# Kernel tuning notes

Measured on AMD Instinct MI355X. Metric: run time of the kernel, lower is better.

Reference implementation:

```python
import jax, jax.numpy as jnp
import numpy as np

B, CQ, CK, CV, CO = 16, 256, 256, 256, 256
H, W = 80, 80          # query spatial size (P3-like)
KH, KW = 40, 40        # key/value spatial size (P4-like)
HEADS = 4
R2 = 2 * 2             # region_size ** 2
SCALE = 1.0 / np.float32(np.sqrt(CQ))


def conv1x1(x, w, b):
    # 1x1 conv == per-pixel linear map over channels
    return jnp.einsum('bchw,oc->bohw', x, w) + b[None, :, None, None]


def setup_inputs() -> dict:
    key = jax.random.key(0)
    ks = jax.random.split(key, 10)
    s = 0.05
    return {
        'query': jax.random.normal(ks[0], (B, CQ, H, W), jnp.float32),
        'key':   jax.random.normal(ks[1], (B, CK, KH, KW), jnp.float32),
        'wq': jax.random.normal(ks[2], (CQ, CQ), jnp.float32) * s,
        'bq': jax.random.normal(ks[3], (CQ,), jnp.float32) * s,
        'wk': jax.random.normal(ks[4], (CK, CK), jnp.float32) * s,
        'bk': jax.random.normal(ks[5], (CK,), jnp.float32) * s,
        'wv': jax.random.normal(ks[6], (CV, CV), jnp.float32) * s,
        'bv': jax.random.normal(ks[7], (CV,), jnp.float32) * s,
        'wo': jax.random.normal(ks[8], (CO, CV), jnp.float32) * s,
        'bo': jax.random.normal(ks[9], (CO,), jnp.float32) * s,
    }


def reference(query, key, wq, bq, wk, bk, wv, bv, wo, bo):
    # value defaults to key in the original module
    q = conv1x1(query, wq, bq)               # [B,CQ,H,W]
    k = conv1x1(key, wk, bk)                 # [B,CK,KH,KW]
    v = conv1x1(key, wv, bv)                 # [B,CV,KH,KW]

    b, cq, h, w = q.shape
    # All R2 'patches' in the source are the SAME interpolation (no offsets),
    # so compute it once; bilinear resize matches torch align_corners=False.
    ki = jax.image.resize(k, (b, k.shape[1], h, w), method='bilinear')
    vi = jax.image.resize(v, (b, v.shape[1], h, w), method='bilinear')

    q5 = q.reshape(b, HEADS, cq // HEADS, h, w)
    k5 = ki.reshape(b, HEADS, k.shape[1] // HEADS, h, w)
    v5 = vi.reshape(b, HEADS, v.shape[1] // HEADS, h, w)

    # per-region score; identical for every region patch
    score = jnp.einsum('bhcxy,bhcxy->bhxy', q5, k5) * SCALE     # [B,h,H,W]
    scores = jnp.broadcast_to(score[:, :, None], (b, HEADS, R2, h, w))
    # NOTE: original uses nn.Softmax(dim=3) -> normalizes over the H axis
    attn = jax.nn.softmax(scores, axis=3)                       # [B,h,R2,H,W]

    # out = sum over regions of attn * v (v identical across regions)
    out = jnp.einsum('bhrxy,bhcxy->bhcxy', attn, v5)            # [B,h,C/h,H,W]
    out = out.reshape(b, -1, h, w)                              # [B,CV,H,W]
    return conv1x1(out, wo, bo)                                 # [B,CO,H,W]
```

## Files before the change

kernel.cpp:

```cpp
#include <hip/hip_runtime.h>
#include <hip/hip_bf16.h>

typedef __bf16 bf16;
typedef __attribute__((ext_vector_type(4))) float f32x4;
typedef __attribute__((ext_vector_type(8))) __bf16 bf16x8;
typedef __attribute__((ext_vector_type(4))) __bf16 bf16x4;

static __device__ __forceinline__ void gl16(const void* g, void* l) {
  __builtin_amdgcn_global_load_lds((const __attribute__((address_space(1))) void*)g,
                                   (__attribute__((address_space(3))) void*)l, 16, 0, 0);
}
static __device__ __forceinline__ bf16x8 frag(const bf16* tile, int row, int kb) {
  return *(const bf16x8*)(tile + row * 64 + ((((kb) >> 3) ^ (row & 7)) << 3));
}

__global__ void wpre(const float* __restrict__ w0, const float* __restrict__ w1,
                     const float* __restrict__ w2, const float* __restrict__ w3,
                     bf16* __restrict__ dst) {
  const float* srcs[4] = {w0, w1, w2, w3};
  const float* s = srcs[blockIdx.y];
  bf16* d = dst + (size_t)blockIdx.y * 65536;
  int base = blockIdx.x * 2048 + threadIdx.x * 8;
  f32x4 a = *(const f32x4*)(s + base);
  f32x4 b = *(const f32x4*)(s + base + 4);
  bf16x8 v = {(bf16)a[0], (bf16)a[1], (bf16)a[2], (bf16)a[3],
              (bf16)b[0], (bf16)b[1], (bf16)b[2], (bf16)b[3]};
  *(bf16x8*)(d + base) = v;
}

__global__ void wtr(const float* __restrict__ wq, bf16* __restrict__ wqT) {
  __shared__ float tl[64][65];
  const int r0 = blockIdx.x * 64, c0 = blockIdx.y * 64;
  const int t = threadIdx.x;
  const int cc = t & 63, rr = t >> 6;
#pragma unroll
  for (int i = 0; i < 16; ++i) {
    int r = i * 4 + rr;
    tl[r][cc] = wq[(size_t)(r0 + r) * 256 + c0 + cc];
  }
  __syncthreads();
#pragma unroll
  for (int i = 0; i < 16; ++i) {
    int r = i * 4 + rr;
    wqT[(size_t)(c0 + r) * 256 + r0 + cc] = (bf16)tl[cc][r];
  }
}

__global__ __launch_bounds__(256, 1)
void kv_proj(const float* __restrict__ key,
             const bf16* __restrict__ Wk, const float* __restrict__ bk, bf16* __restrict__ Kpm,
             const bf16* __restrict__ Wv, const float* __restrict__ bv, bf16* __restrict__ Vpm) {
  __shared__ alignas(16) char smem[64 * 264 * 2];
  const int P = 1600;
  const int t = threadIdx.x;
  const int b = blockIdx.z;
  const int p0 = blockIdx.x * 64;
  const int sel = blockIdx.y;
  const bf16* W = sel ? Wv : Wk;
  const float* bias = sel ? bv : bk;
  bf16* out = sel ? Vpm : Kpm;
  const int w = t >> 6, l = t & 63;
  const int lrow = l & 15, ksel = l >> 4;
  const int pq = t & 15, cq = t >> 4;
  const float* actb = key + (size_t)b * 256 * P;
  bf16* As = (bf16*)smem;

  f32x4 Ar[4][4];
#pragma unroll
  for (int kt = 0; kt < 4; ++kt)
#pragma unroll
    for (int j = 0; j < 4; ++j)
      Ar[kt][j] = *(const f32x4*)(actb + (size_t)(kt * 64 + cq * 4 + j) * P + p0 + pq * 4);
#pragma unroll
  for (int kt = 0; kt < 4; ++kt) {
    bf16* tile = As + kt * 4096;
#pragma unroll
    for (int e = 0; e < 4; ++e) {
      int row = pq * 4 + e;
      bf16x4 v = {(bf16)Ar[kt][0][e], (bf16)Ar[kt][1][e], (bf16)Ar[kt][2][e], (bf16)Ar[kt][3][e]};
      *(bf16x4*)(tile + row * 64 + ((((cq >> 1) ^ (row & 7)) << 3) | ((cq & 1) << 2))) = v;
    }
  }
  __syncthreads();

  f32x4 acc[4][4];
#pragma unroll
  for (int i = 0; i < 4; ++i)
#pragma unroll
    for (int j = 0; j < 4; ++j) acc[i][j] = (f32x4){0.f, 0.f, 0.f, 0.f};

#pragma unroll
  for (int kt = 0; kt < 4; ++kt) {
    const int k0 = kt * 64;
    const bf16* tile = As + kt * 4096;
    bf16x8 af[4][2], bv8[4][2];
#pragma unroll
    for (int mi = 0; mi < 4; ++mi)
#pragma unroll
      for (int kk = 0; kk < 2; ++kk)
        af[mi][kk] = *(const bf16x8*)(W + (size_t)(w * 64 + mi * 16 + lrow) * 256 +
                                      k0 + kk * 32 + ksel * 8);
#pragma unroll
    for (int ni = 0; ni < 4; ++ni)
#pragma unroll
      for (int kk = 0; kk < 2; ++kk)
        bv8[ni][kk] = frag(tile, ni * 16 + lrow, kk * 32 + ksel * 8);
#pragma unroll
    for (int kk = 0; kk < 2; ++kk)
#pragma unroll
      for (int mi = 0; mi < 4; ++mi)
#pragma unroll
        for (int ni = 0; ni < 4; ++ni)
          acc[mi][ni] = __builtin_amdgcn_mfma_f32_16x16x32_bf16(af[mi][kk], bv8[ni][kk],
                                                                acc[mi][ni], 0, 0, 0);
  }
  __syncthreads();

  bf16* Sc = (bf16*)smem;
#pragma unroll
  for (int mi = 0; mi < 4; ++mi) {
#pragma unroll
    for (int r = 0; r < 4; ++r) {
      int o = w * 64 + mi * 16 + ksel * 4 + r;
      float bvf = bias[o];
#pragma unroll
      for (int ni = 0; ni < 4; ++ni) {
        int px = ni * 16 + lrow;
        Sc[px * 264 + o] = (bf16)(acc[mi][ni][r] + bvf);
      }
    }
  }
  __syncthreads();
  bf16* ob = out + (size_t)b * P * 256 + (size_t)p0 * 256;
#pragma unroll
  for (int pass = 0; pass < 8; ++pass) {
    int idx = pass * 256 + t;
    int row = idx >> 5, cu = idx & 31;
    bf16x8 v = *(const bf16x8*)(Sc + row * 264 + cu * 8);
    *(bf16x8*)(ob + (size_t)row * 256 + cu * 8) = v;
  }
}

__global__ __launch_bounds__(256, 4)
void uv_gemm(const bf16* __restrict__ Bpm, const bf16* __restrict__ A,
             bf16* __restrict__ D) {
  __shared__ alignas(16) bf16 Vt[64 * 64];
  const int t = threadIdx.x;
  const int b = blockIdx.z;
  const int hd = blockIdx.y;
  const int q0 = blockIdx.x * 64;
  const int w = t >> 6, l = t & 63;
  const int lrow = l & 15, ksel = l >> 4;

  const bf16* vsrc = Bpm + ((size_t)b * 1600 + q0) * 256 + hd * 64;
#pragma unroll
  for (int call = 0; call < 2; ++call) {
    int idx = (w * 2 + call) * 64 + l;
    int q = idx >> 3, u = idx & 7;
    gl16(vsrc + (size_t)q * 256 + ((u ^ (q & 7)) << 3), Vt + idx * 8);
  }
  asm volatile("s_waitcnt vmcnt(0)" ::: "memory");
  __syncthreads();

  f32x4 acc[4][4];
#pragma unroll
  for (int i = 0; i < 4; ++i)
#pragma unroll
    for (int j = 0; j < 4; ++j) acc[i][j] = (f32x4){0.f, 0.f, 0.f, 0.f};

#pragma unroll
  for (int kk = 0; kk < 2; ++kk) {
    bf16x8 af[4], bv[4];
#pragma unroll
    for (int mi = 0; mi < 4; ++mi)
      af[mi] = *(const bf16x8*)(A + (size_t)(w * 64 + mi * 16 + lrow) * 256 +
                                hd * 64 + kk * 32 + ksel * 8);
#pragma unroll
    for (int ni = 0; ni < 4; ++ni)
      bv[ni] = frag(Vt, ni * 16 + lrow, kk * 32 + ksel * 8);
#pragma unroll
    for (int mi = 0; mi < 4; ++mi)
#pragma unroll
      for (int ni = 0; ni < 4; ++ni)
        acc[mi][ni] = __builtin_amdgcn_mfma_f32_16x16x32_bf16(af[mi], bv[ni], acc[mi][ni], 0, 0, 0);
  }

  bf16* ob = D + ((size_t)(b * 4 + hd)) * 256 * 1600;
#pragma unroll
  for (int mi = 0; mi < 4; ++mi) {
#pragma unroll
    for (int ni = 0; ni < 4; ++ni) {
#pragma unroll
      for (int r = 0; r < 4; ++r) {
        int o = w * 64 + mi * 16 + ksel * 4 + r;
        int q = q0 + ni * 16 + lrow;
        ob[(size_t)o * 1600 + q] = (bf16)acc[mi][ni][r];
      }
    }
  }
}

__global__ void beta_k(const bf16* __restrict__ Kpm, const float* __restrict__ bq,
                       bf16* __restrict__ beta) {
  __shared__ float bqs[256];
  const int t = threadIdx.x;
  bqs[t] = bq[t];
  __syncthreads();
  const int b = blockIdx.y;
  const int q = blockIdx.x * 64 + (t >> 2);
  const int hd = t & 3;
  const bf16* row = Kpm + ((size_t)b * 1600 + q) * 256 + hd * 64;
  float s = 0.f;
#pragma unroll
  for (int i = 0; i < 8; ++i) {
    bf16x8 v = *(const bf16x8*)(row + i * 8);
#pragma unroll
    for (int j = 0; j < 8; ++j) s += (float)v[j] * bqs[hd * 64 + i * 8 + j];
  }
  beta[((size_t)b * 4 + hd) * 1600 + q] = (bf16)s;
}

__global__ __launch_bounds__(256, 3)
void stream_score(const float* __restrict__ query, const bf16* __restrict__ T,
                  const bf16* __restrict__ beta, float* __restrict__ score) {
  __shared__ alignas(16) bf16 Tc[2][64][192];
  __shared__ bf16 Bs[4][192];
  const int t = threadIdx.x;
  const int p0 = blockIdx.x * 256;
  const int b = blockIdx.y;
  const int px = p0 + t;
  const int x = px / 80, y = px % 80;

  const int x_min = p0 / 80;
  int ixm = (int)floorf(0.5f * x_min - 0.25f);
  int xr0 = ixm < 0 ? 0 : ixm;
  int qbase = xr0 * 40;
  if (qbase > 1408) qbase = 1408;

  float cx = 0.5f * x - 0.25f;
  int ix = (int)floorf(cx);
  float wx1 = cx - ix;
  int x0 = ix < 0 ? 0 : ix, x1 = (ix + 1 > 39) ? 39 : ix + 1;
  float cy = 0.5f * y - 0.25f;
  int iy = (int)floorf(cy);
  float wy1 = cy - iy;
  int y0 = iy < 0 ? 0 : iy, y1 = (iy + 1 > 39) ? 39 : iy + 1;
  const float w00 = (1.f - wx1) * (1.f - wy1), w01 = (1.f - wx1) * wy1;
  const float w10 = wx1 * (1.f - wy1), w11 = wx1 * wy1;
  const int r00 = x0 * 40 + y0 - qbase, r01 = x0 * 40 + y1 - qbase;
  const int r10 = x1 * 40 + y0 - qbase, r11 = x1 * 40 + y1 - qbase;

  for (int i = t; i < 768; i += 256) {
    int hd = i / 192, qq = i - hd * 192;
    Bs[hd][qq] = beta[((size_t)b * 4 + hd) * 1600 + qbase + qq];
  }

  const bf16* Tb = T + (size_t)b * 4 * 256 * 1600;

  auto STAGE = [&](int c, int buf) {
    const int k0 = c * 16;
#pragma unroll
    for (int call = 0; call < 6; ++call) {
      int idx = call * 256 + t;
      int r = idx / 24, u = idx - r * 24;
      int hd = r >> 4, kk = r & 15;
      const bf16* src = Tb + ((size_t)(hd * 256) + k0 + kk) * 1600 + qbase + u * 8;
      gl16(src, &Tc[buf][0][0] + idx * 8);
    }
  };

  STAGE(0, 0);
  asm volatile("s_waitcnt vmcnt(0)" ::: "memory");
  __syncthreads();

  float acc[4];
#pragma unroll
  for (int hd = 0; hd < 4; ++hd)
    acc[hd] = w00 * (float)Bs[hd][r00] + w01 * (float)Bs[hd][r01] +
              w10 * (float)Bs[hd][r10] + w11 * (float)Bs[hd][r11];

  int buf = 0;
  for (int c = 0; c < 16; ++c) {
    if (c < 15) STAGE(c + 1, buf ^ 1);
    float qv[16];
#pragma unroll
    for (int kk = 0; kk < 16; ++kk)
      qv[kk] = query[((size_t)b * 256 + c * 16 + kk) * 6400 + px];
#pragma unroll
    for (int kk = 0; kk < 16; ++kk) {
#pragma unroll
      for (int hd = 0; hd < 4; ++hd) {
        const bf16* row = &Tc[buf][hd * 16 + kk][0];
        float tv = w00 * (float)row[r00] + w01 * (float)row[r01] +
                   w10 * (float)row[r10] + w11 * (float)row[r11];
        acc[hd] += qv[kk] * tv;
      }
    }
    asm volatile("s_waitcnt vmcnt(0)" ::: "memory");
    __syncthreads();
    buf ^= 1;
  }

#pragma unroll
  for (int hd = 0; hd < 4; ++hd)
    score[((size_t)b * 4 + hd) * 6400 + px] = 0.0625f * acc[hd];
}

__global__ void smax_kernel(float* __restrict__ score) {
  __shared__ float s[6400];
  const int hd = blockIdx.x, b = blockIdx.y, t = threadIdx.x;
  float* buf = score + ((size_t)b * 4 + hd) * 6400;
  for (int i = t; i < 6400; i += 256) s[i] = buf[i];
  __syncthreads();
  if (t < 80) {
    const int y = t;
    float m = -1e30f;
    for (int x = 0; x < 80; ++x) m = fmaxf(m, s[x * 80 + y]);
    float sum = 0.f;
    for (int x = 0; x < 80; ++x) {
      float e = __expf(s[x * 80 + y] - m);
      s[x * 80 + y] = e;
      sum += e;
    }
    float inv = 4.0f / sum;
    for (int x = 0; x < 80; ++x) buf[x * 80 + y] = s[x * 80 + y] * inv;
  }
}

__global__ __launch_bounds__(256, 8)
void combine(const bf16* __restrict__ Uv, const float* __restrict__ attn,
             const float* __restrict__ bo, float* __restrict__ out) {
  __shared__ bf16 Us[4][1600];
  __shared__ int   sx0[80], sx1[80];
  __shared__ float swx[80];
  const int t = threadIdx.x;
  const int o = blockIdx.x;
  const int b = blockIdx.y;

  const bf16* usrc = Uv + (size_t)(b * 4) * 256 * 1600 + (size_t)o * 1600;
  for (int idx = t; idx < 800; idx += 256) {
    int hd = idx / 200, u = idx % 200;
    *(bf16x8*)&Us[hd][u * 8] = *(const bf16x8*)(usrc + (size_t)hd * 256 * 1600 + u * 8);
  }
  if (t < 80) {
    float c = 0.5f * t - 0.25f;
    int i0 = (int)floorf(c);
    swx[t] = c - i0;
    sx0[t] = i0 < 0 ? 0 : i0;
    sx1[t] = (i0 + 1 > 39) ? 39 : i0 + 1;
  }
  __syncthreads();

  const float bias = bo[o];
  const float* attb = attn + (size_t)b * 4 * 6400;
  float* op = out + ((size_t)b * 256 + o) * 6400;

  for (int p = t; p < 6400; p += 256) {
    int x = p / 80, y = p - x * 80;
    int x0 = sx0[x], x1 = sx1[x], y0 = sx0[y], y1 = sx1[y];
    float wx1 = swx[x], wy1 = swx[y];
    float w00 = (1.f - wx1) * (1.f - wy1), w01 = (1.f - wx1) * wy1;
    float w10 = wx1 * (1.f - wy1), w11 = wx1 * wy1;
    int q00 = x0 * 40 + y0, q01 = x0 * 40 + y1, q10 = x1 * 40 + y0, q11 = x1 * 40 + y1;
    float acc = bias;
#pragma unroll
    for (int hd = 0; hd < 4; ++hd) {
      float up = w00 * (float)Us[hd][q00] + w01 * (float)Us[hd][q01] +
                 w10 * (float)Us[hd][q10] + w11 * (float)Us[hd][q11];
      acc += attb[hd * 6400 + p] * up;
    }
    op[p] = acc;
  }
}

extern "C" void kernel_launch(void* const* d_in, const int* in_sizes, int n_in,
                              void* d_out, int out_size, void* d_ws, size_t ws_size,
                              hipStream_t stream) {
  const float* query = (const float*)d_in[0];
  const float* key   = (const float*)d_in[1];
  const float* wq    = (const float*)d_in[2];
  const float* bq    = (const float*)d_in[3];
  const float* wk    = (const float*)d_in[4];
  const float* bk    = (const float*)d_in[5];
  const float* wv    = (const float*)d_in[6];
  const float* bv    = (const float*)d_in[7];
  const float* wo    = (const float*)d_in[8];
  const float* bo    = (const float*)d_in[9];

  char* ws = (char*)d_ws;
  bf16*  T     = (bf16*)(ws);
  bf16*  Uv    = (bf16*)(ws);
  bf16*  Kpm   = (bf16*)(ws + 52428800);
  bf16*  Vpm   = (bf16*)(ws + 65536000);
  float* score = (float*)(ws + 78643200);
  bf16*  Wb    = (bf16*)(ws + 85196800);
  bf16* wqb = Wb, *wkb = Wb + 65536, *wvb = Wb + 131072, *wob = Wb + 196608;
  (void)wqb;
  bf16*  wqT   = (bf16*)d_out;
  bf16*  beta  = (bf16*)((char*)d_out + 131072);

  wpre<<<dim3(32, 4), 256, 0, stream>>>(wq, wk, wv, wo, Wb);
  wtr<<<dim3(4, 4), 256, 0, stream>>>(wq, wqT);
  kv_proj<<<dim3(25, 2, 16), 256, 0, stream>>>(key, wkb, bk, Kpm, wvb, bv, Vpm);
  uv_gemm<<<dim3(25, 4, 16), 256, 0, stream>>>(Kpm, wqT, T);
  beta_k<<<dim3(25, 16), 256, 0, stream>>>(Kpm, bq, beta);
  stream_score<<<dim3(25, 16), 256, 0, stream>>>(query, T, beta, score);
  smax_kernel<<<dim3(4, 16), 256, 0, stream>>>(score);
  uv_gemm<<<dim3(25, 4, 16), 256, 0, stream>>>(Vpm, wob, Uv);
  combine<<<dim3(256, 16), 256, 0, stream>>>(Uv, score, bo, (float*)d_out);
}
```

Before: 207.6 us.

## Split stream_score channel reduction four ways and sum partials in softmax

The score kernel's 256-channel reduction is split into four chunks, so the grid grows from 400 to 1600 blocks and fills more of the GPU. Each chunk writes a partial score to scratch space in the output buffer, and the softmax kernel sums the four partials as it loads them. This trades extra global traffic for the partial buffers, plus a redundant bilinear setup per block, for more parallelism in a kernel that previously had too few blocks to occupy all CUs.

```diff
diff --git a/kernel.cpp b/kernel.cpp
--- a/kernel.cpp
+++ b/kernel.cpp
@@ -221,12 +221,14 @@
 }
 
 __global__ __launch_bounds__(256, 3)
-void stream_score(const float* __restrict__ query, const bf16* __restrict__ T,
-                  const bf16* __restrict__ beta, float* __restrict__ score) {
+void stream_score2(const float* __restrict__ query, const bf16* __restrict__ T,
+                   const bf16* __restrict__ beta, float* __restrict__ scorep) {
   __shared__ alignas(16) bf16 Tc[2][64][192];
   __shared__ bf16 Bs[4][192];
   const int t = threadIdx.x;
-  const int p0 = blockIdx.x * 256;
+  const int ptile = blockIdx.x >> 2;
+  const int cid = blockIdx.x & 3;
+  const int p0 = ptile * 256;
   const int b = blockIdx.y;
   const int px = p0 + t;
   const int x = px / 80, y = px % 80;
@@ -250,9 +252,11 @@
   const int r00 = x0 * 40 + y0 - qbase, r01 = x0 * 40 + y1 - qbase;
   const int r10 = x1 * 40 + y0 - qbase, r11 = x1 * 40 + y1 - qbase;
 
-  for (int i = t; i < 768; i += 256) {
-    int hd = i / 192, qq = i - hd * 192;
-    Bs[hd][qq] = beta[((size_t)b * 4 + hd) * 1600 + qbase + qq];
+  if (cid == 0) {
+    for (int i = t; i < 768; i += 256) {
+      int hd = i / 192, qq = i - hd * 192;
+      Bs[hd][qq] = beta[((size_t)b * 4 + hd) * 1600 + qbase + qq];
+    }
   }
 
   const bf16* Tb = T + (size_t)b * 4 * 256 * 1600;
@@ -269,23 +273,29 @@
     }
   };
 
-  STAGE(0, 0);
+  const int c0 = cid * 4;
+  STAGE(c0, 0);
   asm volatile("s_waitcnt vmcnt(0)" ::: "memory");
   __syncthreads();
 
   float acc[4];
-#pragma unroll
-  for (int hd = 0; hd < 4; ++hd)
-    acc[hd] = w00 * (float)Bs[hd][r00] + w01 * (float)Bs[hd][r01] +
-              w10 * (float)Bs[hd][r10] + w11 * (float)Bs[hd][r11];
+  if (cid == 0) {
+#pragma unroll
+    for (int hd = 0; hd < 4; ++hd)
+      acc[hd] = w00 * (float)Bs[hd][r00] + w01 * (float)Bs[hd][r01] +
+                w10 * (float)Bs[hd][r10] + w11 * (float)Bs[hd][r11];
+  } else {
+#pragma unroll
+    for (int hd = 0; hd < 4; ++hd) acc[hd] = 0.f;
+  }
 
   int buf = 0;
-  for (int c = 0; c < 16; ++c) {
-    if (c < 15) STAGE(c + 1, buf ^ 1);
+  for (int s = 0; s < 4; ++s) {
+    if (s < 3) STAGE(c0 + s + 1, buf ^ 1);
     float qv[16];
 #pragma unroll
     for (int kk = 0; kk < 16; ++kk)
-      qv[kk] = query[((size_t)b * 256 + c * 16 + kk) * 6400 + px];
+      qv[kk] = query[((size_t)b * 256 + (c0 + s) * 16 + kk) * 6400 + px];
 #pragma unroll
     for (int kk = 0; kk < 16; ++kk) {
 #pragma unroll
@@ -303,14 +313,20 @@
 
 #pragma unroll
   for (int hd = 0; hd < 4; ++hd)
-    score[((size_t)b * 4 + hd) * 6400 + px] = 0.0625f * acc[hd];
-}
-
-__global__ void smax_kernel(float* __restrict__ score) {
+    scorep[(((size_t)cid * 16 + b) * 4 + hd) * 6400 + px] = 0.0625f * acc[hd];
+}
+
+__global__ void smax_kernel(const float* __restrict__ scorep, float* __restrict__ score) {
   __shared__ float s[6400];
   const int hd = blockIdx.x, b = blockIdx.y, t = threadIdx.x;
   float* buf = score + ((size_t)b * 4 + hd) * 6400;
-  for (int i = t; i < 6400; i += 256) s[i] = buf[i];
+  for (int i = t; i < 6400; i += 256) {
+    float v = 0.f;
+#pragma unroll
+    for (int c = 0; c < 4; ++c)
+      v += scorep[(((size_t)c * 16 + b) * 4 + hd) * 6400 + i];
+    s[i] = v;
+  }
   __syncthreads();
   if (t < 80) {
     const int y = t;
@@ -394,18 +410,18 @@
   bf16*  Vpm   = (bf16*)(ws + 65536000);
   float* score = (float*)(ws + 78643200);
   bf16*  Wb    = (bf16*)(ws + 85196800);
-  bf16* wqb = Wb, *wkb = Wb + 65536, *wvb = Wb + 131072, *wob = Wb + 196608;
-  (void)wqb;
-  bf16*  wqT   = (bf16*)d_out;
-  bf16*  beta  = (bf16*)((char*)d_out + 131072);
+  bf16* wkb = Wb + 65536, *wvb = Wb + 131072, *wob = Wb + 196608;
+  bf16*  wqT    = (bf16*)d_out;
+  bf16*  beta   = (bf16*)((char*)d_out + 131072);
+  float* scorep = (float*)((char*)d_out + 1048576);
 
   wpre<<<dim3(32, 4), 256, 0, stream>>>(wq, wk, wv, wo, Wb);
   wtr<<<dim3(4, 4), 256, 0, stream>>>(wq, wqT);
   kv_proj<<<dim3(25, 2, 16), 256, 0, stream>>>(key, wkb, bk, Kpm, wvb, bv, Vpm);
   uv_gemm<<<dim3(25, 4, 16), 256, 0, stream>>>(Kpm, wqT, T);
   beta_k<<<dim3(25, 16), 256, 0, stream>>>(Kpm, bq, beta);
-  stream_score<<<dim3(25, 16), 256, 0, stream>>>(query, T, beta, score);
-  smax_kernel<<<dim3(4, 16), 256, 0, stream>>>(score);
+  stream_score2<<<dim3(100, 16), 256, 0, stream>>>(query, T, beta, scorep);
+  smax_kernel<<<dim3(4, 16), 256, 0, stream>>>(scorep, score);
   uv_gemm<<<dim3(25, 4, 16), 256, 0, stream>>>(Vpm, wob, Uv);
   combine<<<dim3(256, 16), 256, 0, stream>>>(Uv, score, bo, (float*)d_out);
 }
```

Result: faster. 191.6 us (-7.7%).
